# Optimization experiments

Hardware: AMD Instinct MI355X
Metric: run time of the kernel (lower is better)

Reference implementation:

```python
import jax, jax.numpy as jnp
import numpy as np

B, L, D = 256, 512, 512

def setup_inputs() -> dict:
    key = jax.random.key(0)
    k1, k2, k3, k4, k5 = jax.random.split(key, 5)
    scale = 1.0 / np.sqrt(D)  # keep logits in a sane range
    return {
        "text_features": jax.random.normal(k1, (B, L, D), dtype=jnp.float32),
        "image_features": jax.random.normal(k2, (B, D), dtype=jnp.float32),
        "W_ML": jax.random.normal(k3, (D, D), dtype=jnp.float32) * scale,
        "W_MV": jax.random.normal(k4, (D, D), dtype=jnp.float32) * scale,
        "tau": jnp.ones((1,), dtype=jnp.float32),
        "padding_mask": jax.random.randint(k5, (B, L), 0, 2).astype(bool),
    }

def reference(text_features, image_features, W_ML, W_MV, tau, padding_mask):
    b, l, _ = text_features.shape
    tau_c = jnp.clip(tau, 0.001)  # [1]
    valid = ~padding_mask  # [B,L] True where token is real
    # Linear(bias=False): y = x @ W.T
    text_proj = jnp.einsum('bld,ed->ble', text_features, W_ML)   # [B,L,D]
    image_proj = jnp.einsum('bd,ed->be', image_features, W_MV)   # [B,D]
    neg_inf = jnp.float32(-jnp.inf)
    # positive scores: own image vs own text tokens
    s_iji = jnp.einsum('bd,bld->bl', image_proj, text_proj) / tau_c  # [B,L]
    # all-images-vs-text denominator: s_kji[i,l,k] = <text[i,l], image[k]>
    s_kji = jnp.einsum('ild,kd->ilk', text_proj, image_proj) / tau_c  # [B,L,B]
    mask_kj = valid.T[None, :, :]  # [1,L,B] -> valid[k,l] per (i,l,k)
    s_kji = jnp.where(mask_kj, s_kji, neg_inf)
    denom_log = jax.nn.logsumexp(s_kji, axis=2)  # [B,L]
    # cross-batch text negatives: s_iok[i,k,l] = <image[i], text[k,l]>
    s_iok = jnp.einsum('id,kld->ikl', image_proj, text_proj) / tau_c  # [B,B,L]
    mask_ko = valid[None, :, :]  # [1,B,L]
    mask_neq = ~jnp.eye(b, dtype=bool)[:, :, None]  # exclude k == i
    s_iok_f = jnp.where(mask_ko & mask_neq, s_iok, neg_inf).reshape(b, -1)
    cross_log = jax.nn.logsumexp(s_iok_f, axis=1)  # [B]
    neg_log = jnp.logaddexp(s_iji, cross_log[:, None])  # [B,L]
    denom_log = jnp.where(valid, denom_log, 0.0)
    neg_log = jnp.where(valid, neg_log, 0.0)
    f1 = denom_log - s_iji
    f2 = neg_log - s_iji
    loss_mat = 0.5 * (f1 + f2)
    n_valid = jnp.sum(valid)
    loss = jnp.sum(jnp.where(valid, loss_mat, 0.0)) / n_valid
    return loss
```

## Files before the change

kernel.cpp:

```cpp
#include <hip/hip_runtime.h>
#include <math.h>


#define B_ 256
#define L_ 512
#define D_ 512
#define ROWS (B_ * L_)
#define NT (ROWS / 64)
#define NEG_INF (-INFINITY)

typedef __attribute__((ext_vector_type(8))) short s8_t;
typedef __attribute__((ext_vector_type(4))) float f4_t;
typedef __attribute__((ext_vector_type(2))) float f2_t;
typedef __attribute__((ext_vector_type(4))) unsigned short us4_t;

__device__ inline unsigned short f2bf(float x) {
    unsigned int u = __float_as_uint(x);
    u += 0x7FFFu + ((u >> 16) & 1u);
    return (unsigned short)(u >> 16);
}

__global__ __launch_bounds__(256) void ip_kernel(const float* __restrict__ img,
                                                 const float* __restrict__ Wmv,
                                                 float* __restrict__ ip) {
    int kt = blockIdx.x >> 3, et = blockIdx.x & 7;
    __shared__ float Ast[32][36];
    __shared__ float Bst[32][72];
    int tid = threadIdx.x;
    int ty = tid >> 4;
    int tx = tid & 15;
    float acc[2][4] = {};
    int sr = tid >> 3, sc = (tid & 7) * 4;
    for (int d0 = 0; d0 < D_; d0 += 32) {
        f4_t a = *(const f4_t*)(img + (size_t)(kt * 32 + sr) * D_ + d0 + sc);
        f4_t b0 = *(const f4_t*)(Wmv + (size_t)(et * 64 + sr) * D_ + d0 + sc);
        f4_t b1 = *(const f4_t*)(Wmv + (size_t)(et * 64 + sr + 32) * D_ + d0 + sc);
        __syncthreads();
#pragma unroll
        for (int m = 0; m < 4; m++) {
            Ast[sc + m][sr] = a[m];
            Bst[sc + m][sr] = b0[m];
            Bst[sc + m][sr + 32] = b1[m];
        }
        __syncthreads();
#pragma unroll 4
        for (int d = 0; d < 32; d++) {
            f2_t a2 = *(const f2_t*)&Ast[d][ty * 2];
            f4_t b4 = *(const f4_t*)&Bst[d][tx * 4];
#pragma unroll
            for (int i = 0; i < 2; i++)
#pragma unroll
                for (int j = 0; j < 4; j++) acc[i][j] = fmaf(a2[i], b4[j], acc[i][j]);
        }
    }
#pragma unroll
    for (int i = 0; i < 2; i++) {
        f4_t o; o[0] = acc[i][0]; o[1] = acc[i][1]; o[2] = acc[i][2]; o[3] = acc[i][3];
        *(f4_t*)(ip + (size_t)(kt * 32 + ty * 2 + i) * D_ + et * 64 + tx * 4) = o;
    }
}

__global__ __launch_bounds__(256) void c_kernel(const float* __restrict__ ip,
                                                const float* __restrict__ Wml,
                                                const float* __restrict__ tau,
                                                unsigned short* __restrict__ Cb) {
    int kt = blockIdx.x >> 3, dt = blockIdx.x & 7;
    __shared__ float Ast[32][36];
    __shared__ float Bst[32][72];
    int tid = threadIdx.x;
    int ty = tid >> 4;
    int tx = tid & 15;
    float acc[2][4] = {};
    int sr = tid >> 3, sc = (tid & 7) * 4;
    int br = tid >> 4, bc = (tid & 15) * 4;
    for (int e0 = 0; e0 < D_; e0 += 32) {
        f4_t a = *(const f4_t*)(ip + (size_t)(kt * 32 + sr) * D_ + e0 + sc);
        f4_t b0 = *(const f4_t*)(Wml + (size_t)(e0 + br) * D_ + dt * 64 + bc);
        f4_t b1 = *(const f4_t*)(Wml + (size_t)(e0 + br + 16) * D_ + dt * 64 + bc);
        __syncthreads();
#pragma unroll
        for (int m = 0; m < 4; m++) Ast[sc + m][sr] = a[m];
        *(f4_t*)&Bst[br][bc] = b0;
        *(f4_t*)&Bst[br + 16][bc] = b1;
        __syncthreads();
#pragma unroll 4
        for (int e = 0; e < 32; e++) {
            f2_t a2 = *(const f2_t*)&Ast[e][ty * 2];
            f4_t b4 = *(const f4_t*)&Bst[e][tx * 4];
#pragma unroll
            for (int i = 0; i < 2; i++)
#pragma unroll
                for (int j = 0; j < 4; j++) acc[i][j] = fmaf(a2[i], b4[j], acc[i][j]);
        }
    }
    float it = 1.0f / fmaxf(tau[0], 0.001f);
#pragma unroll
    for (int i = 0; i < 2; i++) {
        us4_t o;
#pragma unroll
        for (int j = 0; j < 4; j++) o[j] = f2bf(acc[i][j] * it);
        *(us4_t*)(Cb + (size_t)(kt * 32 + ty * 2 + i) * D_ + dt * 64 + tx * 4) = o;
    }
}

__global__ __launch_bounds__(256) void mask_kernel(const int* __restrict__ pad,
                                                   unsigned long long* __restrict__ mbits) {
    int l = blockIdx.x;
    int w = threadIdx.x >> 6;
    int j = threadIdx.x & 63;
    unsigned long long bal = __ballot(pad[(w * 64 + j) * L_ + l] == 0);
    if (j == 0) mbits[l * 4 + w] = bal;
}

struct StageRegs { f4_t av0, av1; s8_t bv0, bv1, bv2, bv3; };

__device__ __attribute__((always_inline)) inline void g_load(
    const float* aptr, const unsigned short* bptr, int koff, StageRegs& r) {
    r.av0 = *(const f4_t*)(aptr + koff);
    r.av1 = *(const f4_t*)(aptr + koff + 4);
    r.bv0 = *(const s8_t*)(bptr + koff);
    r.bv1 = *(const s8_t*)(bptr + (size_t)64 * D_ + koff);
    r.bv2 = *(const s8_t*)(bptr + (size_t)128 * D_ + koff);
    r.bv3 = *(const s8_t*)(bptr + (size_t)192 * D_ + koff);
}

__device__ __attribute__((always_inline)) inline void lds_store(
    unsigned short* a_s, unsigned short* b_s, int arow, int akq, int bn, int bkq,
    const StageRegs& r) {
    s8_t a8;
    a8[0] = (short)f2bf(r.av0[0]); a8[1] = (short)f2bf(r.av0[1]);
    a8[2] = (short)f2bf(r.av0[2]); a8[3] = (short)f2bf(r.av0[3]);
    a8[4] = (short)f2bf(r.av1[0]); a8[5] = (short)f2bf(r.av1[1]);
    a8[6] = (short)f2bf(r.av1[2]); a8[7] = (short)f2bf(r.av1[3]);
    *(s8_t*)(a_s + arow * 40 + akq * 8) = a8;
    *(s8_t*)(b_s + (bn + 0) * 40 + bkq * 8)   = r.bv0;
    *(s8_t*)(b_s + (bn + 64) * 40 + bkq * 8)  = r.bv1;
    *(s8_t*)(b_s + (bn + 128) * 40 + bkq * 8) = r.bv2;
    *(s8_t*)(b_s + (bn + 192) * 40 + bkq * 8) = r.bv3;
}

__device__ __attribute__((always_inline)) inline void do_mfma(
    const unsigned short* a_s, const unsigned short* b_s, int mm, int qd, int wave,
    f4_t acc[4][4]) {
    s8_t af[4], bf[4];
#pragma unroll
    for (int mt = 0; mt < 4; mt++)
        af[mt] = *(const s8_t*)(a_s + (mt * 16 + mm) * 40 + qd * 8);
#pragma unroll
    for (int nt = 0; nt < 4; nt++)
        bf[nt] = *(const s8_t*)(b_s + (wave * 64 + nt * 16 + mm) * 40 + qd * 8);
#pragma unroll
    for (int mt = 0; mt < 4; mt++)
#pragma unroll
        for (int nt = 0; nt < 4; nt++)
            acc[mt][nt] = __builtin_amdgcn_mfma_f32_16x16x32_bf16(
                af[mt], bf[nt], acc[mt][nt], 0, 0, 0);
}

__global__ __launch_bounds__(256) void gemm_mfma_kernel(
    const float* __restrict__ text, const unsigned short* __restrict__ Cb,
    const unsigned long long* __restrict__ mbits,
    float* __restrict__ denom, float* __restrict__ siji,
    float* __restrict__ crossM, float* __restrict__ crossS) {
    __shared__ __align__(16) float lds[12800];
    unsigned short* A0 = (unsigned short*)lds;
    unsigned short* Bb0 = A0 + 2560;
    unsigned short* A1 = A0 + 12800;
    unsigned short* Bb1 = A1 + 2560;
    float* Sh  = lds;
    float* pm  = lds + 8224;
    float* ps  = lds + 8352;
    float* rvadj = lds + 8480;

    const int tile = blockIdx.x;
    const int row0 = tile * 64;
    const int bIdx = row0 >> 9;
    const int l0 = row0 & 511;
    const int tid = threadIdx.x;
    const int wave = tid >> 6;
    const int lane = tid & 63;
    const int qd = lane >> 4;
    const int mm = lane & 15;

    f4_t acc[4][4];
#pragma unroll
    for (int mt = 0; mt < 4; mt++)
#pragma unroll
        for (int nt = 0; nt < 4; nt++)
#pragma unroll
            for (int r = 0; r < 4; r++) acc[mt][nt][r] = 0.f;

    const int arow = tid >> 2, akq = tid & 3;
    const float* aptr = text + (size_t)(row0 + arow) * D_ + akq * 8;
    const int bkq = tid & 3, bn = tid >> 2;
    const unsigned short* bptr = Cb + (size_t)bn * D_ + bkq * 8;

    StageRegs rg;
    g_load(aptr, bptr, 0, rg);
    lds_store(A0, Bb0, arow, akq, bn, bkq, rg);
#pragma unroll 1
    for (int k0 = 0; k0 < 16; k0 += 2) {
        g_load(aptr, bptr, (k0 + 1) * 32, rg);
        __syncthreads();
        do_mfma(A0, Bb0, mm, qd, wave, acc);
        lds_store(A1, Bb1, arow, akq, bn, bkq, rg);
        bool more = (k0 + 2) < 16;
        if (more) g_load(aptr, bptr, (k0 + 2) * 32, rg);
        __syncthreads();
        do_mfma(A1, Bb1, mm, qd, wave, acc);
        if (more) lds_store(A0, Bb0, arow, akq, bn, bkq, rg);
    }

    float cm = NEG_INF, cs = 0.f;
    const int mw = bIdx >> 6, mb = bIdx & 63;

#pragma unroll
    for (int h = 0; h < 2; h++) {
        __syncthreads();
#pragma unroll
        for (int mt2 = 0; mt2 < 2; mt2++) {
            int mt = h * 2 + mt2;
            int rl = mt2 * 16 + qd * 4;
#pragma unroll
            for (int nt = 0; nt < 4; nt++) {
                int col = wave * 64 + nt * 16 + mm;
#pragma unroll
                for (int r = 0; r < 4; r++)
                    Sh[(rl + r) * 257 + col] = acc[mt][nt][r];
            }
        }
        if (tid < 32) {
            int l = l0 + h * 32 + tid;
            rvadj[tid] = ((mbits[l * 4 + mw] >> mb) & 1ULL) ? 0.f : NEG_INF;
        }
        __syncthreads();

        {
            float m2 = NEG_INF;
#pragma unroll 8
            for (int r = 0; r < 32; r++)
                m2 = fmaxf(m2, Sh[r * 257 + tid] + rvadj[r]);
            if (m2 > NEG_INF) {
                float s2 = 0.f;
#pragma unroll 8
                for (int r = 0; r < 32; r++)
                    s2 += __expf(Sh[r * 257 + tid] + rvadj[r] - m2);
                float M = fmaxf(cm, m2);
                cs = cs * __expf(cm - M) + s2 * __expf(m2 - M);
                cm = M;
            }
        }
        if (tid < 128) {
            int row = tid & 31, grp = tid >> 5;
            int l = l0 + h * 32 + row;
            unsigned long long bits = mbits[l * 4 + grp];
            const float* Srow = Sh + row * 257 + grp * 64;
            float m = NEG_INF;
#pragma unroll 8
            for (int c = 0; c < 64; c++) {
                float adj = ((bits >> c) & 1ULL) ? 0.f : NEG_INF;
                m = fmaxf(m, Srow[c] + adj);
            }
            float s = 0.f;
            if (m > NEG_INF) {
#pragma unroll 8
                for (int c = 0; c < 64; c++) {
                    float adj = ((bits >> c) & 1ULL) ? 0.f : NEG_INF;
                    s += __expf(Srow[c] + adj - m);
                }
            }
            pm[grp * 32 + row] = m;
            ps[grp * 32 + row] = s;
        }
        __syncthreads();
        if (tid < 32) {
            float m0 = pm[tid], m1 = pm[32 + tid], m2 = pm[64 + tid], m3 = pm[96 + tid];
            float M = fmaxf(fmaxf(m0, m1), fmaxf(m2, m3));
            float dl;
            if (M == NEG_INF) dl = NEG_INF;
            else {
                float s = ps[tid] * __expf(m0 - M) + ps[32 + tid] * __expf(m1 - M) +
                          ps[64 + tid] * __expf(m2 - M) + ps[96 + tid] * __expf(m3 - M);
                dl = M + __logf(s);
            }
            int gr = row0 + h * 32 + tid;
            denom[gr] = dl;
            siji[gr] = Sh[tid * 257 + bIdx];
        }
    }
    if (tid == bIdx) { cm = NEG_INF; cs = 0.f; }
    crossM[(size_t)tid * NT + tile] = cm;
    crossS[(size_t)tid * NT + tile] = cs;
}

__global__ __launch_bounds__(256) void cross_combine_kernel(const float* __restrict__ crossM,
                                                            const float* __restrict__ crossS,
                                                            float* __restrict__ crossLog) {
    int i = blockIdx.x;
    int tid = threadIdx.x;
    float m = NEG_INF, s = 0.f;
    for (int e = 0; e < NT / 256; e++) {
        int t = e * 256 + tid;
        float m2 = crossM[(size_t)i * NT + t];
        float s2 = crossS[(size_t)i * NT + t];
        if (m2 > NEG_INF) {
            if (m == NEG_INF) { m = m2; s = s2; }
            else {
                float M = fmaxf(m, m2);
                s = s * expf(m - M) + s2 * expf(m2 - M);
                m = M;
            }
        }
    }
    __shared__ float sm[256], ss[256];
    sm[tid] = m; ss[tid] = s;
    __syncthreads();
    for (int off = 128; off > 0; off >>= 1) {
        if (tid < off) {
            float m1 = sm[tid], s1 = ss[tid];
            float m2 = sm[tid + off], s2 = ss[tid + off];
            float M = fmaxf(m1, m2);
            float sv;
            if (M == NEG_INF) sv = 0.f;
            else sv = s1 * expf(m1 - M) + s2 * expf(m2 - M);
            sm[tid] = M; ss[tid] = sv;
        }
        __syncthreads();
    }
    if (tid == 0) crossLog[i] = (sm[0] == NEG_INF) ? NEG_INF : sm[0] + logf(ss[0]);
}

__global__ __launch_bounds__(256) void loss_partial_kernel(
    const int* __restrict__ pad, const float* __restrict__ denom,
    const float* __restrict__ siji, const float* __restrict__ crossLog,
    float* __restrict__ psum, float* __restrict__ pcnt) {
    int tid = threadIdx.x;
    int idx = blockIdx.x * 256 + tid;
    float term = 0.f, cnt = 0.f;
    if (pad[idx] == 0) {
        float dl = denom[idx], sv = siji[idx], cl = crossLog[idx >> 9];
        float M = fmaxf(sv, cl);
        float neg = M + log1pf(expf(-fabsf(sv - cl)));
        term = 0.5f * (dl + neg) - sv;
        cnt = 1.f;
    }
    __shared__ float bs[256], bc[256];
    bs[tid] = term; bc[tid] = cnt;
    __syncthreads();
    for (int off = 128; off > 0; off >>= 1) {
        if (tid < off) { bs[tid] += bs[tid + off]; bc[tid] += bc[tid + off]; }
        __syncthreads();
    }
    if (tid == 0) { psum[blockIdx.x] = bs[0]; pcnt[blockIdx.x] = bc[0]; }
}

__global__ __launch_bounds__(256) void final_kernel(const float* __restrict__ psum,
                                                    const float* __restrict__ pcnt,
                                                    float* __restrict__ out) {
    int tid = threadIdx.x;
    __shared__ float bs[256], bc[256];
    bs[tid] = psum[tid] + psum[tid + 256];
    bc[tid] = pcnt[tid] + pcnt[tid + 256];
    __syncthreads();
    for (int off = 128; off > 0; off >>= 1) {
        if (tid < off) { bs[tid] += bs[tid + off]; bc[tid] += bc[tid + off]; }
        __syncthreads();
    }
    if (tid == 0) out[0] = bs[0] / bc[0];
}

extern "C" void kernel_launch(void* const* d_in, const int* in_sizes, int n_in,
                              void* d_out, int out_size, void* d_ws, size_t ws_size,
                              hipStream_t stream) {
    (void)in_sizes; (void)n_in; (void)out_size; (void)ws_size;
    const float* text = (const float*)d_in[0];
    const float* img  = (const float*)d_in[1];
    const float* Wml  = (const float*)d_in[2];
    const float* Wmv  = (const float*)d_in[3];
    const float* tau  = (const float*)d_in[4];
    const int* pad    = (const int*)d_in[5];
    float* out = (float*)d_out;

    float* ws = (float*)d_ws;
    float* ip       = ws;
    unsigned short* Cb = (unsigned short*)(ws + 131072);
    unsigned long long* mbits = (unsigned long long*)(ws + 262144);
    float* denom    = ws + 266240;
    float* siji     = ws + 397312;
    float* crossM   = ws + 528384;
    float* crossS   = ws + 1052672;
    float* crossLog = ws + 1576960;
    float* psum     = ws + 1577216;
    float* pcnt     = ws + 1577728;

    hipLaunchKernelGGL(ip_kernel,   dim3(64),  dim3(256), 0, stream, img, Wmv, ip);
    hipLaunchKernelGGL(c_kernel,    dim3(64),  dim3(256), 0, stream, ip, Wml, tau, Cb);
    hipLaunchKernelGGL(mask_kernel, dim3(L_),  dim3(256), 0, stream, pad, mbits);
    hipLaunchKernelGGL(gemm_mfma_kernel, dim3(NT), dim3(256), 0, stream,
                       text, Cb, mbits, denom, siji, crossM, crossS);
    hipLaunchKernelGGL(cross_combine_kernel, dim3(B_), dim3(256), 0, stream,
                       crossM, crossS, crossLog);
    hipLaunchKernelGGL(loss_partial_kernel, dim3(ROWS / 256), dim3(256), 0, stream,
                       pad, denom, siji, crossLog, psum, pcnt);
    hipLaunchKernelGGL(final_kernel, dim3(1), dim3(256), 0, stream, psum, pcnt, out);
}
```

Before: 496.2 us.

## Load GEMM operands directly to registers, drop LDS staging, use 128-thread blocks

The text-by-image GEMM no longer stages A and B tiles through shared memory. Each of two waves loads its A rows from global memory and converts them to bf16 in registers. B is read straight from global memory in a new k-major interleaved layout that c_kernel now writes, so each lane's MFMA fragment is one contiguous 16-byte load. Blocks shrink to 128 threads, each wave covering 32 rows by all 256 columns, and the epilogue is adjusted so each thread handles two column groups. This removes LDS traffic and the per-stage barriers, at the cost of many more accumulator registers and B being fetched redundantly by every wave through cache.

New measurement: 544.7 us. 1.1x slower.

```diff
diff --git a/kernel.cpp b/kernel.cpp
--- a/kernel.cpp
+++ b/kernel.cpp
@@ -63,7 +63,7 @@
 __global__ __launch_bounds__(256) void c_kernel(const float* __restrict__ ip,
                                                 const float* __restrict__ Wml,
                                                 const float* __restrict__ tau,
-                                                unsigned short* __restrict__ Cb) {
+                                                unsigned short* __restrict__ Cb2) {
     int kt = blockIdx.x >> 3, dt = blockIdx.x & 7;
     __shared__ float Ast[32][36];
     __shared__ float Bst[32][72];
@@ -99,7 +99,9 @@
         us4_t o;
 #pragma unroll
         for (int j = 0; j < 4; j++) o[j] = f2bf(acc[i][j] * it);
-        *(us4_t*)(Cb + (size_t)(kt * 32 + ty * 2 + i) * D_ + dt * 64 + tx * 4) = o;
+        int n = kt * 32 + ty * 2 + i;
+        int kk0 = dt * 64 + tx * 4;
+        *(us4_t*)(Cb2 + (size_t)((kk0 >> 3) * 256 + n) * 8 + (kk0 & 7)) = o;
     }
 }
 
@@ -112,64 +114,15 @@
     if (j == 0) mbits[l * 4 + w] = bal;
 }
 
-struct StageRegs { f4_t av0, av1; s8_t bv0, bv1, bv2, bv3; };
-
-__device__ __attribute__((always_inline)) inline void g_load(
-    const float* aptr, const unsigned short* bptr, int koff, StageRegs& r) {
-    r.av0 = *(const f4_t*)(aptr + koff);
-    r.av1 = *(const f4_t*)(aptr + koff + 4);
-    r.bv0 = *(const s8_t*)(bptr + koff);
-    r.bv1 = *(const s8_t*)(bptr + (size_t)64 * D_ + koff);
-    r.bv2 = *(const s8_t*)(bptr + (size_t)128 * D_ + koff);
-    r.bv3 = *(const s8_t*)(bptr + (size_t)192 * D_ + koff);
-}
-
-__device__ __attribute__((always_inline)) inline void lds_store(
-    unsigned short* a_s, unsigned short* b_s, int arow, int akq, int bn, int bkq,
-    const StageRegs& r) {
-    s8_t a8;
-    a8[0] = (short)f2bf(r.av0[0]); a8[1] = (short)f2bf(r.av0[1]);
-    a8[2] = (short)f2bf(r.av0[2]); a8[3] = (short)f2bf(r.av0[3]);
-    a8[4] = (short)f2bf(r.av1[0]); a8[5] = (short)f2bf(r.av1[1]);
-    a8[6] = (short)f2bf(r.av1[2]); a8[7] = (short)f2bf(r.av1[3]);
-    *(s8_t*)(a_s + arow * 40 + akq * 8) = a8;
-    *(s8_t*)(b_s + (bn + 0) * 40 + bkq * 8)   = r.bv0;
-    *(s8_t*)(b_s + (bn + 64) * 40 + bkq * 8)  = r.bv1;
-    *(s8_t*)(b_s + (bn + 128) * 40 + bkq * 8) = r.bv2;
-    *(s8_t*)(b_s + (bn + 192) * 40 + bkq * 8) = r.bv3;
-}
-
-__device__ __attribute__((always_inline)) inline void do_mfma(
-    const unsigned short* a_s, const unsigned short* b_s, int mm, int qd, int wave,
-    f4_t acc[4][4]) {
-    s8_t af[4], bf[4];
-#pragma unroll
-    for (int mt = 0; mt < 4; mt++)
-        af[mt] = *(const s8_t*)(a_s + (mt * 16 + mm) * 40 + qd * 8);
-#pragma unroll
-    for (int nt = 0; nt < 4; nt++)
-        bf[nt] = *(const s8_t*)(b_s + (wave * 64 + nt * 16 + mm) * 40 + qd * 8);
-#pragma unroll
-    for (int mt = 0; mt < 4; mt++)
-#pragma unroll
-        for (int nt = 0; nt < 4; nt++)
-            acc[mt][nt] = __builtin_amdgcn_mfma_f32_16x16x32_bf16(
-                af[mt], bf[nt], acc[mt][nt], 0, 0, 0);
-}
-
-__global__ __launch_bounds__(256) void gemm_mfma_kernel(
-    const float* __restrict__ text, const unsigned short* __restrict__ Cb,
+__global__ __launch_bounds__(128, 2) void gemm_mfma_kernel(
+    const float* __restrict__ text, const unsigned short* __restrict__ Cb2,
     const unsigned long long* __restrict__ mbits,
     float* __restrict__ denom, float* __restrict__ siji,
     float* __restrict__ crossM, float* __restrict__ crossS) {
-    __shared__ __align__(16) float lds[12800];
-    unsigned short* A0 = (unsigned short*)lds;
-    unsigned short* Bb0 = A0 + 2560;
-    unsigned short* A1 = A0 + 12800;
-    unsigned short* Bb1 = A1 + 2560;
-    float* Sh  = lds;
-    float* pm  = lds + 8224;
-    float* ps  = lds + 8352;
+    __shared__ __align__(16) float lds[8512];
+    float* Sh    = lds;
+    float* pm    = lds + 8224;
+    float* ps    = lds + 8352;
     float* rvadj = lds + 8480;
 
     const int tile = blockIdx.x;
@@ -182,52 +135,81 @@
     const int qd = lane >> 4;
     const int mm = lane & 15;
 
-    f4_t acc[4][4];
-#pragma unroll
-    for (int mt = 0; mt < 4; mt++)
-#pragma unroll
-        for (int nt = 0; nt < 4; nt++)
+    f4_t acc[2][16];
+#pragma unroll
+    for (int mt = 0; mt < 2; mt++)
+#pragma unroll
+        for (int nt = 0; nt < 16; nt++)
 #pragma unroll
             for (int r = 0; r < 4; r++) acc[mt][nt][r] = 0.f;
 
-    const int arow = tid >> 2, akq = tid & 3;
-    const float* aptr = text + (size_t)(row0 + arow) * D_ + akq * 8;
-    const int bkq = tid & 3, bn = tid >> 2;
-    const unsigned short* bptr = Cb + (size_t)bn * D_ + bkq * 8;
-
-    StageRegs rg;
-    g_load(aptr, bptr, 0, rg);
-    lds_store(A0, Bb0, arow, akq, bn, bkq, rg);
+    const int wrow = row0 + wave * 32;
+    const float* aB0 = text + (size_t)(wrow + mm) * D_ + qd * 8;
+    const float* aB1 = aB0 + 16 * D_;
+    const unsigned short* bB = Cb2 + qd * 2048 + mm * 8;
+
+    f4_t ar[4];
+    s8_t aa[2];
+    s8_t bcur[8], bnxt[8];
+
+#define LOAD_A(t) do { \
+        ar[0] = *(const f4_t*)(aB0 + (t) * 32); \
+        ar[1] = *(const f4_t*)(aB0 + (t) * 32 + 4); \
+        ar[2] = *(const f4_t*)(aB1 + (t) * 32); \
+        ar[3] = *(const f4_t*)(aB1 + (t) * 32 + 4); \
+    } while (0)
+#define LOAD_BH(dst, t, half) do { \
+        _Pragma("unroll") \
+        for (int nt = 0; nt < 8; nt++) \
+            dst[nt] = *(const s8_t*)(bB + (t) * 8192 + (half) * 1024 + nt * 128); \
+    } while (0)
+
+    LOAD_A(0);
+    LOAD_BH(bcur, 0, 0);
 #pragma unroll 1
-    for (int k0 = 0; k0 < 16; k0 += 2) {
-        g_load(aptr, bptr, (k0 + 1) * 32, rg);
-        __syncthreads();
-        do_mfma(A0, Bb0, mm, qd, wave, acc);
-        lds_store(A1, Bb1, arow, akq, bn, bkq, rg);
-        bool more = (k0 + 2) < 16;
-        if (more) g_load(aptr, bptr, (k0 + 2) * 32, rg);
-        __syncthreads();
-        do_mfma(A1, Bb1, mm, qd, wave, acc);
-        if (more) lds_store(A0, Bb0, arow, akq, bn, bkq, rg);
-    }
-
-    float cm = NEG_INF, cs = 0.f;
+    for (int t = 0; t < 16; t++) {
+        LOAD_BH(bnxt, t, 1);
+#pragma unroll
+        for (int q = 0; q < 2; q++) {
+            s8_t a8;
+#pragma unroll
+            for (int j = 0; j < 4; j++) {
+                a8[j]     = (short)f2bf(ar[2 * q][j]);
+                a8[j + 4] = (short)f2bf(ar[2 * q + 1][j]);
+            }
+            aa[q] = a8;
+        }
+        int tn = (t + 1) & 15;
+        LOAD_A(tn);
+#pragma unroll
+        for (int nt = 0; nt < 8; nt++) {
+            acc[0][nt] = __builtin_amdgcn_mfma_f32_16x16x32_bf16(aa[0], bcur[nt], acc[0][nt], 0, 0, 0);
+            acc[1][nt] = __builtin_amdgcn_mfma_f32_16x16x32_bf16(aa[1], bcur[nt], acc[1][nt], 0, 0, 0);
+        }
+        LOAD_BH(bcur, tn, 0);
+#pragma unroll
+        for (int nt = 0; nt < 8; nt++) {
+            acc[0][8 + nt] = __builtin_amdgcn_mfma_f32_16x16x32_bf16(aa[0], bnxt[nt], acc[0][8 + nt], 0, 0, 0);
+            acc[1][8 + nt] = __builtin_amdgcn_mfma_f32_16x16x32_bf16(aa[1], bnxt[nt], acc[1][8 + nt], 0, 0, 0);
+        }
+    }
+#undef LOAD_A
+#undef LOAD_BH
+
+    float cm0 = NEG_INF, cs0 = 0.f, cm1 = NEG_INF, cs1 = 0.f;
     const int mw = bIdx >> 6, mb = bIdx & 63;
 
 #pragma unroll
     for (int h = 0; h < 2; h++) {
         __syncthreads();
-#pragma unroll
-        for (int mt2 = 0; mt2 < 2; mt2++) {
-            int mt = h * 2 + mt2;
-            int rl = mt2 * 16 + qd * 4;
-#pragma unroll
-            for (int nt = 0; nt < 4; nt++) {
-                int col = wave * 64 + nt * 16 + mm;
-#pragma unroll
-                for (int r = 0; r < 4; r++)
-                    Sh[(rl + r) * 257 + col] = acc[mt][nt][r];
-            }
+        if (wave == h) {
+#pragma unroll
+            for (int mt = 0; mt < 2; mt++)
+#pragma unroll
+                for (int nt = 0; nt < 16; nt++)
+#pragma unroll
+                    for (int r = 0; r < 4; r++)
+                        Sh[(mt * 16 + qd * 4 + r) * 257 + nt * 16 + mm] = acc[mt][nt][r];
         }
         if (tid < 32) {
             int l = l0 + h * 32 + tid;
@@ -236,21 +218,33 @@
         __syncthreads();
 
         {
-            float m2 = NEG_INF;
+            float m2 = NEG_INF, m3 = NEG_INF;
 #pragma unroll 8
-            for (int r = 0; r < 32; r++)
-                m2 = fmaxf(m2, Sh[r * 257 + tid] + rvadj[r]);
+            for (int r = 0; r < 32; r++) {
+                float adj = rvadj[r];
+                m2 = fmaxf(m2, Sh[r * 257 + tid] + adj);
+                m3 = fmaxf(m3, Sh[r * 257 + 128 + tid] + adj);
+            }
             if (m2 > NEG_INF) {
                 float s2 = 0.f;
 #pragma unroll 8
                 for (int r = 0; r < 32; r++)
                     s2 += __expf(Sh[r * 257 + tid] + rvadj[r] - m2);
-                float M = fmaxf(cm, m2);
-                cs = cs * __expf(cm - M) + s2 * __expf(m2 - M);
-                cm = M;
-            }
-        }
-        if (tid < 128) {
+                float M = fmaxf(cm0, m2);
+                cs0 = cs0 * __expf(cm0 - M) + s2 * __expf(m2 - M);
+                cm0 = M;
+            }
+            if (m3 > NEG_INF) {
+                float s3 = 0.f;
+#pragma unroll 8
+                for (int r = 0; r < 32; r++)
+                    s3 += __expf(Sh[r * 257 + 128 + tid] + rvadj[r] - m3);
+                float M = fmaxf(cm1, m3);
+                cs1 = cs1 * __expf(cm1 - M) + s3 * __expf(m3 - M);
+                cm1 = M;
+            }
+        }
+        {
             int row = tid & 31, grp = tid >> 5;
             int l = l0 + h * 32 + row;
             unsigned long long bits = mbits[l * 4 + grp];
@@ -274,13 +268,13 @@
         }
         __syncthreads();
         if (tid < 32) {
-            float m0 = pm[tid], m1 = pm[32 + tid], m2 = pm[64 + tid], m3 = pm[96 + tid];
-            float M = fmaxf(fmaxf(m0, m1), fmaxf(m2, m3));
+            float m0v = pm[tid], m1v = pm[32 + tid], m2v = pm[64 + tid], m3v = pm[96 + tid];
+            float M = fmaxf(fmaxf(m0v, m1v), fmaxf(m2v, m3v));
             float dl;
             if (M == NEG_INF) dl = NEG_INF;
             else {
-                float s = ps[tid] * __expf(m0 - M) + ps[32 + tid] * __expf(m1 - M) +
-                          ps[64 + tid] * __expf(m2 - M) + ps[96 + tid] * __expf(m3 - M);
+                float s = ps[tid] * __expf(m0v - M) + ps[32 + tid] * __expf(m1v - M) +
+                          ps[64 + tid] * __expf(m2v - M) + ps[96 + tid] * __expf(m3v - M);
                 dl = M + __logf(s);
             }
             int gr = row0 + h * 32 + tid;
@@ -288,9 +282,12 @@
             siji[gr] = Sh[tid * 257 + bIdx];
         }
     }
-    if (tid == bIdx) { cm = NEG_INF; cs = 0.f; }
-    crossM[(size_t)tid * NT + tile] = cm;
-    crossS[(size_t)tid * NT + tile] = cs;
+    if (tid == bIdx)       { cm0 = NEG_INF; cs0 = 0.f; }
+    if (tid + 128 == bIdx) { cm1 = NEG_INF; cs1 = 0.f; }
+    crossM[(size_t)tid * NT + tile] = cm0;
+    crossS[(size_t)tid * NT + tile] = cs0;
+    crossM[(size_t)(tid + 128) * NT + tile] = cm1;
+    crossS[(size_t)(tid + 128) * NT + tile] = cs1;
 }
 
 __global__ __launch_bounds__(256) void cross_combine_kernel(const float* __restrict__ crossM,
@@ -383,7 +380,7 @@
 
     float* ws = (float*)d_ws;
     float* ip       = ws;
-    unsigned short* Cb = (unsigned short*)(ws + 131072);
+    unsigned short* Cb2 = (unsigned short*)(ws + 131072);
     unsigned long long* mbits = (unsigned long long*)(ws + 262144);
     float* denom    = ws + 266240;
     float* siji     = ws + 397312;
@@ -394,10 +391,10 @@
     float* pcnt     = ws + 1577728;
 
     hipLaunchKernelGGL(ip_kernel,   dim3(64),  dim3(256), 0, stream, img, Wmv, ip);
-    hipLaunchKernelGGL(c_kernel,    dim3(64),  dim3(256), 0, stream, ip, Wml, tau, Cb);
+    hipLaunchKernelGGL(c_kernel,    dim3(64),  dim3(256), 0, stream, ip, Wml, tau, Cb2);
     hipLaunchKernelGGL(mask_kernel, dim3(L_),  dim3(256), 0, stream, pad, mbits);
-    hipLaunchKernelGGL(gemm_mfma_kernel, dim3(NT), dim3(256), 0, stream,
-                       text, Cb, mbits, denom, siji, crossM, crossS);
+    hipLaunchKernelGGL(gemm_mfma_kernel, dim3(NT), dim3(128), 0, stream,
+                       text, Cb2, mbits, denom, siji, crossM, crossS);
     hipLaunchKernelGGL(cross_combine_kernel, dim3(B_), dim3(256), 0, stream,
                        crossM, crossS, crossLog);
     hipLaunchKernelGGL(loss_partial_kernel, dim3(ROWS / 256), dim3(256), 0, stream,
```
